# Kernel optimization log

Measured on AMD Instinct MI355X. Metric: run time of the kernel, lower is better.

Reference implementation:

```python
import jax, jax.numpy as jnp
import numpy as np

D_IN = 1024
D_OUT = 1024


def setup_inputs() -> dict:
    key = jax.random.key(0)
    k_x, k_q, k_k, k_v = jax.random.split(key, 4)
    x = jax.random.normal(k_x, (8, 2048, D_IN), dtype=jnp.float32)
    s = 1.0 / np.sqrt(D_IN)
    W_query = jax.random.uniform(k_q, (D_IN, D_OUT), jnp.float32, -s, s)
    W_key = jax.random.uniform(k_k, (D_IN, D_OUT), jnp.float32, -s, s)
    W_value = jax.random.uniform(k_v, (D_IN, D_OUT), jnp.float32, -s, s)
    return {"x": x, "W_query": W_query, "W_key": W_key, "W_value": W_value}


def reference(x, W_query, W_key, W_value):
    # x: [B, N, d_in]; weights stored as [d_in, d_out] (already transposed vs torch Linear)
    B, N, _ = x.shape
    q = x @ W_query          # [B, N, d_out]
    k = x @ W_key
    v = x @ W_value
    scores = jnp.einsum('bnd,bmd->bnm', q, k)  # [B, N, N]
    causal = jnp.tril(jnp.ones((N, N), dtype=bool))
    scores = jnp.where(causal, scores, -jnp.inf)
    weights = jax.nn.softmax(scores / np.sqrt(D_OUT), axis=-1)
    # dropout p=0.0 -> identity
    return jnp.einsum('bnm,bmd->bnd', weights, v)
```

## Files before the change

kernel.cpp:

```cpp
#include <hip/hip_runtime.h>
#include <hip/hip_bf16.h>

typedef unsigned short u16;
typedef unsigned int u32;
typedef __bf16 bf16x8 __attribute__((ext_vector_type(8)));
typedef float f32x4 __attribute__((ext_vector_type(4)));
typedef unsigned int u32x4 __attribute__((ext_vector_type(4)));

#define BATCH 8
#define SEQ   2048
#define DIM   1024
#define M_TOT (BATCH * SEQ)
#define N_QKV (3 * DIM)

#define OFF_QKV  ((size_t)0)
#define OFF_VT   ((size_t)100663296)
#define OFF_C    ((size_t)134217728)
#define OFF_XB   OFF_C
#define OFF_WT   (OFF_C + (size_t)33554432)
#define OFF_S    OFF_C

__device__ __forceinline__ u16 f32_to_bf16(float f) {
    u32 u = __builtin_bit_cast(u32, f);
    u = (u + 0x7fffu + ((u >> 16) & 1u)) >> 16;
    return (u16)u;
}

__device__ __forceinline__ float bf16_to_f32(u16 h) {
    u32 u = ((u32)h) << 16;
    return __builtin_bit_cast(float, u);
}

__device__ __forceinline__ bf16x8 lds_load8(const u16* p) {
    return __builtin_bit_cast(bf16x8, *(const u32x4*)p);
}

__device__ __forceinline__ void stage_tile64(const u16* gA, size_t lda, u16* ldsA, int tid) {
    int wv = tid >> 6;
#pragma unroll
    for (int iss = 0; iss < 4; ++iss) {
        int s = iss * 256 + tid;
        int row = s >> 3;
        int kg = (s & 7) ^ (row & 7);
        const u16* gp = gA + (size_t)row * lda + (kg << 3);
        u16* lp = ldsA + (size_t)(iss * 256 + wv * 64) * 8;
        __builtin_amdgcn_global_load_lds((const __attribute__((address_space(1))) void*)gp,
                                         (__attribute__((address_space(3))) void*)lp,
                                         16, 0, 0);
    }
}

__device__ __forceinline__ void mfma_step64(const u16* ldsA, const u16* ldsB, int tid,
                                            f32x4 acc[4][4]) {
    int lane = tid & 63;
    int wv = tid >> 6;
    int wr = (wv >> 1) * 64, wc = (wv & 1) * 64;
    int lrow = lane & 15, kgl = lane >> 4;
    int xr = lrow & 7;
#pragma unroll
    for (int ks = 0; ks < 2; ++ks) {
        int off = ((ks * 4 + kgl) ^ xr) << 3;
        bf16x8 a[4], b[4];
#pragma unroll
        for (int i = 0; i < 4; ++i) {
            a[i] = lds_load8(&ldsA[(wr + i * 16 + lrow) * 64 + off]);
            b[i] = lds_load8(&ldsB[(wc + i * 16 + lrow) * 64 + off]);
        }
#pragma unroll
        for (int i = 0; i < 4; ++i)
#pragma unroll
            for (int j = 0; j < 4; ++j)
                acc[i][j] = __builtin_amdgcn_mfma_f32_16x16x32_bf16(a[i], b[j], acc[i][j], 0, 0, 0);
    }
}

__global__ __launch_bounds__(256) void cast_x_kernel(const float* __restrict__ x,
                                                     u16* __restrict__ xb) {
    size_t g = (size_t)blockIdx.x * 256 + threadIdx.x;
    f32x4 v = ((const f32x4*)x)[g];
    u16 o[4] = {f32_to_bf16(v.x), f32_to_bf16(v.y), f32_to_bf16(v.z), f32_to_bf16(v.w)};
    *(unsigned long long*)(xb + g * 4) = *(const unsigned long long*)o;
}

__global__ __launch_bounds__(256) void transpose_w_kernel(const float* __restrict__ wq,
                                                          const float* __restrict__ wk,
                                                          const float* __restrict__ wv,
                                                          u16* __restrict__ wt) {
    __shared__ __align__(16) u16 tile[64][80];
    const float* w = blockIdx.z == 0 ? wq : (blockIdx.z == 1 ? wk : wv);
    int k0 = blockIdx.x * 64, n0 = blockIdx.y * 64;
    for (int g = threadIdx.x; g < 1024; g += 256) {
        int r = g >> 4, c = (g & 15) << 2;
        f32x4 v = *(const f32x4*)(w + (size_t)(k0 + r) * 1024 + n0 + c);
        tile[r][c + 0] = f32_to_bf16(v.x);
        tile[r][c + 1] = f32_to_bf16(v.y);
        tile[r][c + 2] = f32_to_bf16(v.z);
        tile[r][c + 3] = f32_to_bf16(v.w);
    }
    __syncthreads();
    u16* out = wt + (size_t)blockIdx.z * 1024 * 1024;
    for (int g = threadIdx.x; g < 512; g += 256) {
        int nr = g >> 3, kc = (g & 7) << 3;
        __align__(16) u16 tmp[8];
#pragma unroll
        for (int i = 0; i < 8; ++i) tmp[i] = tile[kc + i][nr];
        *(u32x4*)(out + (size_t)(n0 + nr) * 1024 + k0 + kc) = *(const u32x4*)tmp;
    }
}

__global__ __launch_bounds__(256, 2) void gemm_qkv_kernel(const u16* __restrict__ xb,
                                                          const u16* __restrict__ wt,
                                                          u16* __restrict__ qkv) {
    __shared__ __align__(16) u16 ldsA[128 * 64];
    __shared__ __align__(16) u16 ldsB[128 * 64];
    int nt = blockIdx.x, mt = blockIdx.y;
    const u16* A = xb + (size_t)mt * 128 * 1024;
    const u16* B = wt + (size_t)nt * 128 * 1024;
    int tid = threadIdx.x;
    f32x4 acc[4][4] = {};
    for (int kt = 0; kt < 16; ++kt) {
        __syncthreads();
        stage_tile64(A + kt * 64, 1024, ldsA, tid);
        stage_tile64(B + kt * 64, 1024, ldsB, tid);
        __syncthreads();
        mfma_step64(ldsA, ldsB, tid, acc);
    }
    int lane = tid & 63, wv = tid >> 6;
    int wr = (wv >> 1) * 64, wc = (wv & 1) * 64;
    int r0 = (lane >> 4) * 4, c0 = lane & 15;
    size_t mbase = (size_t)mt * 128;
    int nbase = nt * 128;
#pragma unroll
    for (int i = 0; i < 4; ++i)
#pragma unroll
        for (int j = 0; j < 4; ++j) {
            int col = nbase + wc + j * 16 + c0;
            float scale = (col < 1024) ? 0.03125f : 1.0f;
#pragma unroll
            for (int r = 0; r < 4; ++r) {
                int row = wr + i * 16 + r0 + r;
                qkv[(mbase + row) * (size_t)N_QKV + col] = f32_to_bf16(acc[i][j][r] * scale);
            }
        }
}

__global__ __launch_bounds__(256) void transpose_v_kernel(const u16* __restrict__ qkv,
                                                          u16* __restrict__ vt) {
    __shared__ __align__(16) u16 tile[64][80];
    int m0 = blockIdx.x * 64, d0 = blockIdx.y * 64, b = blockIdx.z;
    const u16* src = qkv + (size_t)b * SEQ * N_QKV + 2048;
    for (int g = threadIdx.x; g < 512; g += 256) {
        int r = g >> 3, c = (g & 7) << 3;
        *(u32x4*)&tile[r][c] = *(const u32x4*)(src + (size_t)(m0 + r) * N_QKV + d0 + c);
    }
    __syncthreads();
    u16* dst = vt + (size_t)b * DIM * SEQ;
    for (int g = threadIdx.x; g < 512; g += 256) {
        int dr = g >> 3, mc = (g & 7) << 3;
        __align__(16) u16 tmp[8];
#pragma unroll
        for (int i = 0; i < 8; ++i) tmp[i] = tile[mc + i][dr];
        *(u32x4*)(dst + (size_t)(d0 + dr) * SEQ + m0 + mc) = *(const u32x4*)tmp;
    }
}

__global__ __launch_bounds__(256, 2) void gemm_scores_kernel(const u16* __restrict__ qkv,
                                                             u16* __restrict__ S) {
    int t = blockIdx.x;
    int b = blockIdx.y;
    int ntile = (int)((sqrtf(8.0f * (float)t + 1.0f) - 1.0f) * 0.5f);
    while ((ntile + 1) * (ntile + 2) / 2 <= t) ++ntile;
    while (ntile * (ntile + 1) / 2 > t) --ntile;
    int mtile = t - ntile * (ntile + 1) / 2;
    __shared__ __align__(16) u16 ldsA[128 * 64];
    __shared__ __align__(16) u16 ldsB[128 * 64];
    const u16* A = qkv + (size_t)b * SEQ * N_QKV + (size_t)ntile * 128 * N_QKV;
    const u16* B = qkv + (size_t)b * SEQ * N_QKV + (size_t)mtile * 128 * N_QKV + 1024;
    int tid = threadIdx.x;
    f32x4 acc[4][4] = {};
    for (int kt = 0; kt < 16; ++kt) {
        __syncthreads();
        stage_tile64(A + kt * 64, N_QKV, ldsA, tid);
        stage_tile64(B + kt * 64, N_QKV, ldsB, tid);
        __syncthreads();
        mfma_step64(ldsA, ldsB, tid, acc);
    }
    u16* out = S + (size_t)b * SEQ * SEQ + (size_t)ntile * 128 * SEQ + (size_t)mtile * 128;
    int lane = tid & 63, wv = tid >> 6;
    int wr = (wv >> 1) * 64, wc = (wv & 1) * 64;
    int r0 = (lane >> 4) * 4, c0 = lane & 15;
#pragma unroll
    for (int i = 0; i < 4; ++i)
#pragma unroll
        for (int j = 0; j < 4; ++j) {
            int col = wc + j * 16 + c0;
#pragma unroll
            for (int r = 0; r < 4; ++r) {
                int row = wr + i * 16 + r0 + r;
                out[(size_t)row * SEQ + col] = f32_to_bf16(acc[i][j][r]);
            }
        }
}

__global__ __launch_bounds__(256) void softmax_kernel(u16* __restrict__ SP) {
    int gr = blockIdx.x;
    int n = gr & 2047;
    u16* s = SP + (size_t)gr * SEQ;
    __shared__ float red[4];
    int t = threadIdx.x;
    int base = t << 3;
    int len = n + 1;
    float v[8];
    float lmax = -3.0e38f;
    if (base < len) {
        u32x4 raw = *(const u32x4*)(s + base);
        const u16* h = (const u16*)&raw;
#pragma unroll
        for (int i = 0; i < 8; ++i) {
            v[i] = (base + i < len) ? bf16_to_f32(h[i]) : -3.0e38f;
            lmax = fmaxf(lmax, v[i]);
        }
    } else {
#pragma unroll
        for (int i = 0; i < 8; ++i) v[i] = -3.0e38f;
    }
#pragma unroll
    for (int off = 32; off; off >>= 1) lmax = fmaxf(lmax, __shfl_xor(lmax, off, 64));
    if ((t & 63) == 0) red[t >> 6] = lmax;
    __syncthreads();
    float gmax = fmaxf(fmaxf(red[0], red[1]), fmaxf(red[2], red[3]));
    __syncthreads();
    float lsum = 0.f;
#pragma unroll
    for (int i = 0; i < 8; ++i) {
        float e = __expf(v[i] - gmax);
        v[i] = e;
        lsum += e;
    }
#pragma unroll
    for (int off = 32; off; off >>= 1) lsum += __shfl_xor(lsum, off, 64);
    if ((t & 63) == 0) red[t >> 6] = lsum;
    __syncthreads();
    float inv = 1.0f / (red[0] + red[1] + red[2] + red[3]);
    __align__(16) u16 o[8];
#pragma unroll
    for (int i = 0; i < 8; ++i) o[i] = f32_to_bf16(v[i] * inv);
    *(u32x4*)(s + base) = *(const u32x4*)o;
}

__global__ __launch_bounds__(256, 2) void gemm_out_kernel(const u16* __restrict__ P,
                                                          const u16* __restrict__ vt,
                                                          float* __restrict__ O) {
    __shared__ __align__(16) u16 ldsA[128 * 64];
    __shared__ __align__(16) u16 ldsB[128 * 64];
    int dt = blockIdx.x, b = blockIdx.z;
    int ntile = (SEQ / 128 - 1) - blockIdx.y;
    const u16* A = P + (size_t)b * SEQ * SEQ + (size_t)ntile * 128 * SEQ;
    const u16* B = vt + (size_t)b * DIM * SEQ + (size_t)dt * 128 * SEQ;
    int tid = threadIdx.x;
    f32x4 acc[4][4] = {};
    int kTiles = ntile * 2 + 2;
    for (int kt = 0; kt < kTiles; ++kt) {
        __syncthreads();
        stage_tile64(A + kt * 64, SEQ, ldsA, tid);
        stage_tile64(B + kt * 64, SEQ, ldsB, tid);
        __syncthreads();
        mfma_step64(ldsA, ldsB, tid, acc);
    }
    float* out = O + (size_t)b * SEQ * DIM + (size_t)ntile * 128 * DIM + (size_t)dt * 128;
    int lane = tid & 63, wv = tid >> 6;
    int wr = (wv >> 1) * 64, wc = (wv & 1) * 64;
    int r0 = (lane >> 4) * 4, c0 = lane & 15;
#pragma unroll
    for (int i = 0; i < 4; ++i)
#pragma unroll
        for (int j = 0; j < 4; ++j) {
            int col = wc + j * 16 + c0;
#pragma unroll
            for (int r = 0; r < 4; ++r) {
                int row = wr + i * 16 + r0 + r;
                out[(size_t)row * DIM + col] = acc[i][j][r];
            }
        }
}

extern "C" void kernel_launch(void* const* d_in, const int* in_sizes, int n_in,
                              void* d_out, int out_size, void* d_ws, size_t ws_size,
                              hipStream_t stream) {
    const float* x = (const float*)d_in[0];
    const float* wq = (const float*)d_in[1];
    const float* wk = (const float*)d_in[2];
    const float* wv = (const float*)d_in[3];
    char* ws = (char*)d_ws;
    u16* qkv = (u16*)(ws + OFF_QKV);
    u16* vt = (u16*)(ws + OFF_VT);
    u16* xb = (u16*)(ws + OFF_XB);
    u16* wt = (u16*)(ws + OFF_WT);
    u16* S = (u16*)(ws + OFF_S);
    float* O = (float*)d_out;

    cast_x_kernel<<<M_TOT * DIM / 4 / 256, 256, 0, stream>>>(x, xb);
    transpose_w_kernel<<<dim3(16, 16, 3), 256, 0, stream>>>(wq, wk, wv, wt);
    gemm_qkv_kernel<<<dim3(N_QKV / 128, M_TOT / 128), 256, 0, stream>>>(xb, wt, qkv);
    transpose_v_kernel<<<dim3(SEQ / 64, DIM / 64, BATCH), 256, 0, stream>>>(qkv, vt);
    gemm_scores_kernel<<<dim3(136, BATCH), 256, 0, stream>>>(qkv, S);
    softmax_kernel<<<BATCH * SEQ, 256, 0, stream>>>(S);
    gemm_out_kernel<<<dim3(DIM / 128, SEQ / 128, BATCH), 256, 0, stream>>>(S, vt, O);
}
```

Measured before the change: 398.7 us.

## Use two-wave 128x128 GEMM blocks and merge weight transpose with x cast

```diff
diff --git a/kernel.cpp b/kernel.cpp
--- a/kernel.cpp
+++ b/kernel.cpp
@@ -38,57 +38,63 @@
 __device__ __forceinline__ void stage_tile64(const u16* gA, size_t lda, u16* ldsA, int tid) {
     int wv = tid >> 6;
 #pragma unroll
-    for (int iss = 0; iss < 4; ++iss) {
-        int s = iss * 256 + tid;
+    for (int iss = 0; iss < 8; ++iss) {
+        int s = iss * 128 + tid;
         int row = s >> 3;
         int kg = (s & 7) ^ (row & 7);
         const u16* gp = gA + (size_t)row * lda + (kg << 3);
-        u16* lp = ldsA + (size_t)(iss * 256 + wv * 64) * 8;
+        u16* lp = ldsA + (size_t)(iss * 128 + wv * 64) * 8;
         __builtin_amdgcn_global_load_lds((const __attribute__((address_space(1))) void*)gp,
                                          (__attribute__((address_space(3))) void*)lp,
                                          16, 0, 0);
     }
 }
 
-__device__ __forceinline__ void mfma_step64(const u16* ldsA, const u16* ldsB, int tid,
-                                            f32x4 acc[4][4]) {
+__device__ __forceinline__ void mfma_step2w(const u16* ldsA, const u16* ldsB, int tid,
+                                            f32x4 acc[4][8]) {
     int lane = tid & 63;
     int wv = tid >> 6;
-    int wr = (wv >> 1) * 64, wc = (wv & 1) * 64;
+    int wr = wv * 64;
     int lrow = lane & 15, kgl = lane >> 4;
     int xr = lrow & 7;
 #pragma unroll
     for (int ks = 0; ks < 2; ++ks) {
         int off = ((ks * 4 + kgl) ^ xr) << 3;
-        bf16x8 a[4], b[4];
-#pragma unroll
-        for (int i = 0; i < 4; ++i) {
+        bf16x8 a[4], b[8];
+#pragma unroll
+        for (int i = 0; i < 4; ++i)
             a[i] = lds_load8(&ldsA[(wr + i * 16 + lrow) * 64 + off]);
-            b[i] = lds_load8(&ldsB[(wc + i * 16 + lrow) * 64 + off]);
-        }
+#pragma unroll
+        for (int j = 0; j < 8; ++j)
+            b[j] = lds_load8(&ldsB[(j * 16 + lrow) * 64 + off]);
 #pragma unroll
         for (int i = 0; i < 4; ++i)
 #pragma unroll
-            for (int j = 0; j < 4; ++j)
+            for (int j = 0; j < 8; ++j)
                 acc[i][j] = __builtin_amdgcn_mfma_f32_16x16x32_bf16(a[i], b[j], acc[i][j], 0, 0, 0);
     }
 }
 
-__global__ __launch_bounds__(256) void cast_x_kernel(const float* __restrict__ x,
-                                                     u16* __restrict__ xb) {
-    size_t g = (size_t)blockIdx.x * 256 + threadIdx.x;
-    f32x4 v = ((const f32x4*)x)[g];
-    u16 o[4] = {f32_to_bf16(v.x), f32_to_bf16(v.y), f32_to_bf16(v.z), f32_to_bf16(v.w)};
-    *(unsigned long long*)(xb + g * 4) = *(const unsigned long long*)o;
-}
-
-__global__ __launch_bounds__(256) void transpose_w_kernel(const float* __restrict__ wq,
-                                                          const float* __restrict__ wk,
-                                                          const float* __restrict__ wv,
-                                                          u16* __restrict__ wt) {
+__global__ __launch_bounds__(256) void prep_kernel(const float* __restrict__ x,
+                                                   const float* __restrict__ wq,
+                                                   const float* __restrict__ wk,
+                                                   const float* __restrict__ wv,
+                                                   u16* __restrict__ xb,
+                                                   u16* __restrict__ wt) {
     __shared__ __align__(16) u16 tile[64][80];
-    const float* w = blockIdx.z == 0 ? wq : (blockIdx.z == 1 ? wk : wv);
-    int k0 = blockIdx.x * 64, n0 = blockIdx.y * 64;
+    int blk = blockIdx.x;
+    if (blk >= 768) {
+        size_t g = (size_t)(blk - 768) * 256 + threadIdx.x;
+        f32x4 v = ((const f32x4*)x)[g];
+        u16 o[4] = {f32_to_bf16(v.x), f32_to_bf16(v.y), f32_to_bf16(v.z), f32_to_bf16(v.w)};
+        *(unsigned long long*)(xb + g * 4) = *(const unsigned long long*)o;
+        return;
+    }
+    int z = blk >> 8;
+    int rem = blk & 255;
+    int kt = rem >> 4, nt2 = rem & 15;
+    const float* w = z == 0 ? wq : (z == 1 ? wk : wv);
+    int k0 = kt * 64, n0 = nt2 * 64;
     for (int g = threadIdx.x; g < 1024; g += 256) {
         int r = g >> 4, c = (g & 15) << 2;
         f32x4 v = *(const f32x4*)(w + (size_t)(k0 + r) * 1024 + n0 + c);
@@ -98,7 +104,7 @@
         tile[r][c + 3] = f32_to_bf16(v.w);
     }
     __syncthreads();
-    u16* out = wt + (size_t)blockIdx.z * 1024 * 1024;
+    u16* out = wt + (size_t)z * 1024 * 1024;
     for (int g = threadIdx.x; g < 512; g += 256) {
         int nr = g >> 3, kc = (g & 7) << 3;
         __align__(16) u16 tmp[8];
@@ -108,33 +114,33 @@
     }
 }
 
-__global__ __launch_bounds__(256, 2) void gemm_qkv_kernel(const u16* __restrict__ xb,
-                                                          const u16* __restrict__ wt,
-                                                          u16* __restrict__ qkv) {
+__global__ __launch_bounds__(128) void gemm_qkv_kernel(const u16* __restrict__ xb,
+                                                       const u16* __restrict__ wt,
+                                                       u16* __restrict__ qkv) {
     __shared__ __align__(16) u16 ldsA[128 * 64];
     __shared__ __align__(16) u16 ldsB[128 * 64];
     int nt = blockIdx.x, mt = blockIdx.y;
     const u16* A = xb + (size_t)mt * 128 * 1024;
     const u16* B = wt + (size_t)nt * 128 * 1024;
     int tid = threadIdx.x;
-    f32x4 acc[4][4] = {};
+    f32x4 acc[4][8] = {};
     for (int kt = 0; kt < 16; ++kt) {
         __syncthreads();
         stage_tile64(A + kt * 64, 1024, ldsA, tid);
         stage_tile64(B + kt * 64, 1024, ldsB, tid);
         __syncthreads();
-        mfma_step64(ldsA, ldsB, tid, acc);
+        mfma_step2w(ldsA, ldsB, tid, acc);
     }
     int lane = tid & 63, wv = tid >> 6;
-    int wr = (wv >> 1) * 64, wc = (wv & 1) * 64;
+    int wr = wv * 64;
     int r0 = (lane >> 4) * 4, c0 = lane & 15;
     size_t mbase = (size_t)mt * 128;
     int nbase = nt * 128;
 #pragma unroll
     for (int i = 0; i < 4; ++i)
 #pragma unroll
-        for (int j = 0; j < 4; ++j) {
-            int col = nbase + wc + j * 16 + c0;
+        for (int j = 0; j < 8; ++j) {
+            int col = nbase + j * 16 + c0;
             float scale = (col < 1024) ? 0.03125f : 1.0f;
 #pragma unroll
             for (int r = 0; r < 4; ++r) {
@@ -164,8 +170,8 @@
     }
 }
 
-__global__ __launch_bounds__(256, 2) void gemm_scores_kernel(const u16* __restrict__ qkv,
-                                                             u16* __restrict__ S) {
+__global__ __launch_bounds__(128) void gemm_scores_kernel(const u16* __restrict__ qkv,
+                                                          u16* __restrict__ S) {
     int t = blockIdx.x;
     int b = blockIdx.y;
     int ntile = (int)((sqrtf(8.0f * (float)t + 1.0f) - 1.0f) * 0.5f);
@@ -177,23 +183,23 @@
     const u16* A = qkv + (size_t)b * SEQ * N_QKV + (size_t)ntile * 128 * N_QKV;
     const u16* B = qkv + (size_t)b * SEQ * N_QKV + (size_t)mtile * 128 * N_QKV + 1024;
     int tid = threadIdx.x;
-    f32x4 acc[4][4] = {};
+    f32x4 acc[4][8] = {};
     for (int kt = 0; kt < 16; ++kt) {
         __syncthreads();
         stage_tile64(A + kt * 64, N_QKV, ldsA, tid);
         stage_tile64(B + kt * 64, N_QKV, ldsB, tid);
         __syncthreads();
-        mfma_step64(ldsA, ldsB, tid, acc);
+        mfma_step2w(ldsA, ldsB, tid, acc);
     }
     u16* out = S + (size_t)b * SEQ * SEQ + (size_t)ntile * 128 * SEQ + (size_t)mtile * 128;
     int lane = tid & 63, wv = tid >> 6;
-    int wr = (wv >> 1) * 64, wc = (wv & 1) * 64;
+    int wr = wv * 64;
     int r0 = (lane >> 4) * 4, c0 = lane & 15;
 #pragma unroll
     for (int i = 0; i < 4; ++i)
 #pragma unroll
-        for (int j = 0; j < 4; ++j) {
-            int col = wc + j * 16 + c0;
+        for (int j = 0; j < 8; ++j) {
+            int col = j * 16 + c0;
 #pragma unroll
             for (int r = 0; r < 4; ++r) {
                 int row = wr + i * 16 + r0 + r;
@@ -248,9 +254,9 @@
     *(u32x4*)(s + base) = *(const u32x4*)o;
 }
 
-__global__ __launch_bounds__(256, 2) void gemm_out_kernel(const u16* __restrict__ P,
-                                                          const u16* __restrict__ vt,
-                                                          float* __restrict__ O) {
+__global__ __launch_bounds__(128) void gemm_out_kernel(const u16* __restrict__ P,
+                                                       const u16* __restrict__ vt,
+                                                       float* __restrict__ O) {
     __shared__ __align__(16) u16 ldsA[128 * 64];
     __shared__ __align__(16) u16 ldsB[128 * 64];
     int dt = blockIdx.x, b = blockIdx.z;
@@ -258,24 +264,24 @@
     const u16* A = P + (size_t)b * SEQ * SEQ + (size_t)ntile * 128 * SEQ;
     const u16* B = vt + (size_t)b * DIM * SEQ + (size_t)dt * 128 * SEQ;
     int tid = threadIdx.x;
-    f32x4 acc[4][4] = {};
+    f32x4 acc[4][8] = {};
     int kTiles = ntile * 2 + 2;
     for (int kt = 0; kt < kTiles; ++kt) {
         __syncthreads();
         stage_tile64(A + kt * 64, SEQ, ldsA, tid);
         stage_tile64(B + kt * 64, SEQ, ldsB, tid);
         __syncthreads();
-        mfma_step64(ldsA, ldsB, tid, acc);
+        mfma_step2w(ldsA, ldsB, tid, acc);
     }
     float* out = O + (size_t)b * SEQ * DIM + (size_t)ntile * 128 * DIM + (size_t)dt * 128;
     int lane = tid & 63, wv = tid >> 6;
-    int wr = (wv >> 1) * 64, wc = (wv & 1) * 64;
+    int wr = wv * 64;
     int r0 = (lane >> 4) * 4, c0 = lane & 15;
 #pragma unroll
     for (int i = 0; i < 4; ++i)
 #pragma unroll
-        for (int j = 0; j < 4; ++j) {
-            int col = wc + j * 16 + c0;
+        for (int j = 0; j < 8; ++j) {
+            int col = j * 16 + c0;
 #pragma unroll
             for (int r = 0; r < 4; ++r) {
                 int row = wr + i * 16 + r0 + r;
@@ -299,11 +305,10 @@
     u16* S = (u16*)(ws + OFF_S);
     float* O = (float*)d_out;
 
-    cast_x_kernel<<<M_TOT * DIM / 4 / 256, 256, 0, stream>>>(x, xb);
-    transpose_w_kernel<<<dim3(16, 16, 3), 256, 0, stream>>>(wq, wk, wv, wt);
-    gemm_qkv_kernel<<<dim3(N_QKV / 128, M_TOT / 128), 256, 0, stream>>>(xb, wt, qkv);
+    prep_kernel<<<768 + M_TOT * DIM / 4 / 256, 256, 0, stream>>>(x, wq, wk, wv, xb, wt);
+    gemm_qkv_kernel<<<dim3(N_QKV / 128, M_TOT / 128), 128, 0, stream>>>(xb, wt, qkv);
     transpose_v_kernel<<<dim3(SEQ / 64, DIM / 64, BATCH), 256, 0, stream>>>(qkv, vt);
-    gemm_scores_kernel<<<dim3(136, BATCH), 256, 0, stream>>>(qkv, S);
+    gemm_scores_kernel<<<dim3(136, BATCH), 128, 0, stream>>>(qkv, S);
     softmax_kernel<<<BATCH * SEQ, 256, 0, stream>>>(S);
-    gemm_out_kernel<<<dim3(DIM / 128, SEQ / 128, BATCH), 256, 0, stream>>>(S, vt, O);
-}
+    gemm_out_kernel<<<dim3(DIM / 128, SEQ / 128, BATCH), 128, 0, stream>>>(S, vt, O);
+}
```

New measurement: 502.7 us. 1.26x slower.
